# Performance work log

Hardware: AMD Instinct MI355X
Metric: run time of the kernel (lower is better)

## Reference

```python
import jax, jax.numpy as jnp
import numpy as np

B, L, D_MODEL = 4, 2048, 512
N_HEAD, D_K, D_V = 8, 64, 64
RANK = 20


def tt_linear(x, g1, g2, g3, g4, b):
    # TT-matrix linear: input modes (4,4,8,4), output modes (4,4,8,4), ranks [1,20,20,20,1]
    Bx, Lx, _ = x.shape
    t = x.reshape(Bx * Lx, 4, 4, 8, 4)
    t = jnp.einsum('bwxyz,wou->bxyzou', t, g1[0])        # g1: [1,m1,n1,r1]
    t = jnp.einsum('bxyzou,uxpv->byzopv', t, g2)         # g2: [r1,m2,n2,r2]
    t = jnp.einsum('byzopv,vyqw->bzopqw', t, g3)         # g3: [r2,m3,n3,r3]
    t = jnp.einsum('bzopqw,wzs->bopqs', t, g4[..., 0])   # g4: [r3,m4,n4,1]
    return t.reshape(Bx, Lx, -1) + b


def setup_inputs() -> dict:
    key = jax.random.key(0)
    ks = jax.random.split(key, 8)
    scale = jnp.float32(0.15)
    inp = {}
    for name, kk in zip(['wq', 'wk', 'wv', 'fc'], ks[:4]):
        sub = jax.random.split(kk, 4)
        inp[name + '_g1'] = jax.random.normal(sub[0], (1, 4, 4, RANK), jnp.float32) * scale
        inp[name + '_g2'] = jax.random.normal(sub[1], (RANK, 4, 4, RANK), jnp.float32) * scale
        inp[name + '_g3'] = jax.random.normal(sub[2], (RANK, 8, 8, RANK), jnp.float32) * scale
        inp[name + '_g4'] = jax.random.normal(sub[3], (RANK, 4, 4, 1), jnp.float32) * scale
        inp[name + '_b'] = jnp.zeros((D_MODEL,), jnp.float32)
    inp['q'] = jax.random.normal(ks[4], (B, L, D_MODEL), jnp.float32)
    inp['k'] = jax.random.normal(ks[5], (B, L, D_MODEL), jnp.float32)
    inp['v'] = jax.random.normal(ks[6], (B, L, D_MODEL), jnp.float32)
    inp['ln_g'] = jnp.ones((D_MODEL,), jnp.float32)
    inp['ln_b'] = jnp.zeros((D_MODEL,), jnp.float32)
    return inp


def reference(q, k, v,
              wq_g1, wq_g2, wq_g3, wq_g4, wq_b,
              wk_g1, wk_g2, wk_g3, wk_g4, wk_b,
              wv_g1, wv_g2, wv_g3, wv_g4, wv_b,
              fc_g1, fc_g2, fc_g3, fc_g4, fc_b,
              ln_g, ln_b):
    Bx, Lq, _ = q.shape
    residual = q
    qh = tt_linear(q, wq_g1, wq_g2, wq_g3, wq_g4, wq_b).reshape(Bx, Lq, N_HEAD, D_K).transpose(0, 2, 1, 3)
    kh = tt_linear(k, wk_g1, wk_g2, wk_g3, wk_g4, wk_b).reshape(Bx, Lq, N_HEAD, D_K).transpose(0, 2, 1, 3)
    vh = tt_linear(v, wv_g1, wv_g2, wv_g3, wv_g4, wv_b).reshape(Bx, Lq, N_HEAD, D_V).transpose(0, 2, 1, 3)
    temp = jnp.sqrt(jnp.float32(D_K))
    attn = jnp.einsum('bhqd,bhkd->bhqk', qh / temp, kh)  # explicit [B,H,L,L] scores
    attn = jax.nn.softmax(attn, axis=-1)
    o = jnp.einsum('bhqk,bhkd->bhqd', attn, vh)
    o = o.transpose(0, 2, 1, 3).reshape(Bx, Lq, N_HEAD * D_V)
    out = tt_linear(o, fc_g1, fc_g2, fc_g3, fc_g4, fc_b) + residual
    mu = out.mean(-1, keepdims=True)
    var = out.var(-1, keepdims=True)
    out = (out - mu) / jnp.sqrt(var + 1e-12) * ln_g + ln_b
    return (out, attn)
```

## Files before the change

### kernel.cpp

```cpp
#include <hip/hip_runtime.h>
#include <hip/hip_bf16.h>
#include <math.h>

#define BB 4
#define LL 2048
#define DM 512
#define NH 8
#define DK 64
#define RANK 20

typedef __attribute__((ext_vector_type(8))) short short8;
typedef __attribute__((ext_vector_type(4))) short short4b;
typedef __attribute__((ext_vector_type(4))) float f32x4;
typedef __hip_bfloat16 bf16;

__device__ inline short to_bf(float x) {
    bf16 h = __float2bfloat16(x);
    return *reinterpret_cast<short*>(&h);
}
__device__ inline unsigned pk2(float lo, float hi) {
    return ((unsigned)(unsigned short)to_bf(hi) << 16) |
           (unsigned)(unsigned short)to_bf(lo);
}

struct BwArgs {
    const float* g1[4]; const float* g2[4]; const float* g3[4]; const float* g4[4];
    bf16* wt[4];
};
__global__ __launch_bounds__(256) void build_w_kernel(BwArgs args)
{
    int s4 = blockIdx.y;
    const float* __restrict__ g1 = args.g1[s4];
    const float* __restrict__ g2 = args.g2[s4];
    const float* __restrict__ g3 = args.g3[s4];
    const float* __restrict__ g4 = args.g4[s4];
    bf16* __restrict__ Wt = args.wt[s4];

    int idx = blockIdx.x * 256 + threadIdx.x;
    if (idx >= 4*4*8*4*4*8) return;
    int q = idx & 7; int t = idx >> 3;
    int p = t & 3;  t >>= 2;
    int o = t & 3;  t >>= 2;
    int y = t & 7;  t >>= 3;
    int x = t & 3;  t >>= 2;
    int w = t & 3;

    float c[RANK];
    for (int v = 0; v < RANK; ++v) c[v] = 0.f;
    for (int u = 0; u < RANK; ++u) {
        float a = g1[(w*4 + o)*RANK + u];
        const float* g2p = g2 + ((u*4 + x)*4 + p)*RANK;
        for (int v = 0; v < RANK; ++v) c[v] += a * g2p[v];
    }
    float d[RANK];
    for (int r = 0; r < RANK; ++r) d[r] = 0.f;
    for (int v = 0; v < RANK; ++v) {
        float cv = c[v];
        const float* g3p = g3 + ((v*8 + y)*8 + q)*RANK;
        for (int r = 0; r < RANK; ++r) d[r] += cv * g3p[r];
    }
    for (int z = 0; z < 4; ++z) {
        for (int s = 0; s < 4; ++s) {
            float acc = 0.f;
            for (int r = 0; r < RANK; ++r) acc += d[r] * g4[(r*4 + z)*4 + s];
            int i = ((w*4 + x)*8 + y)*4 + z;
            int j = ((o*4 + p)*8 + q)*4 + s;
            Wt[(size_t)j*DM + i] = __float2bfloat16(acc);
        }
    }
}

struct CvtArgs { const float* src[3]; bf16* dst[3]; };
__global__ __launch_bounds__(256) void cvt_kernel(CvtArgs args)
{
    int a = blockIdx.y;
    const float* __restrict__ s = args.src[a];
    bf16* __restrict__ d = args.dst[a];
    size_t i = ((size_t)blockIdx.x * 256 + threadIdx.x) * 8;
    float4 v0 = *(const float4*)&s[i];
    float4 v1 = *(const float4*)&s[i + 4];
    short8 h;
    h[0] = to_bf(v0.x); h[1] = to_bf(v0.y); h[2] = to_bf(v0.z); h[3] = to_bf(v0.w);
    h[4] = to_bf(v1.x); h[5] = to_bf(v1.y); h[6] = to_bf(v1.z); h[7] = to_bf(v1.w);
    *(short8*)&d[i] = h;
}

#define GEMM_CORE64(Ap, Bp)                                                        \
    f32x4 acc[2][2] = {};                                                          \
    for (int k0 = 0; k0 < DM; k0 += 32) {                                          \
        short8 a[2], b[2];                                                         \
        _Pragma("unroll")                                                          \
        for (int mt = 0; mt < 2; ++mt)                                             \
            a[mt] = *(const short8*)&Ap[(size_t)(mt*16 + l15)*DM + k0 + l4*8];     \
        _Pragma("unroll")                                                          \
        for (int nt = 0; nt < 2; ++nt)                                             \
            b[nt] = *(const short8*)&Bp[(size_t)(nt*16 + l15)*DM + k0 + l4*8];     \
        _Pragma("unroll")                                                          \
        for (int mt = 0; mt < 2; ++mt)                                             \
            _Pragma("unroll")                                                      \
            for (int nt = 0; nt < 2; ++nt)                                         \
                acc[mt][nt] = __builtin_amdgcn_mfma_f32_16x16x32_bf16(             \
                    a[mt], b[nt], acc[mt][nt], 0, 0, 0);                           \
    }

struct QkvArgs {
    const bf16* A[3]; const bf16* W[3]; const float* bias[3];
    bf16* outQ; bf16* outK; bf16* outV;
};
__global__ __launch_bounds__(256) void gemm_qkv_kernel(QkvArgs args)
{
    int z = blockIdx.z;
    const bf16* __restrict__ A  = args.A[z];
    const bf16* __restrict__ Wt = args.W[z];
    const float* __restrict__ bias = args.bias[z];

    int m0 = blockIdx.x * 64, n0 = blockIdx.y * 64;
    int t = threadIdx.x, lane = t & 63, wave = t >> 6;
    int l15 = lane & 15, l4 = lane >> 4;
    int wm = wave >> 1, wn = wave & 1;
    const bf16* Ap = A  + (size_t)(m0 + wm*32)*DM;
    const bf16* Bp = Wt + (size_t)(n0 + wn*32)*DM;

    GEMM_CORE64(Ap, Bp)

    if (z < 2) {
        bf16* __restrict__ out = (z == 0) ? args.outQ : args.outK;
        float oscale = (z == 0) ? 0.18033688f : 1.0f;
        #pragma unroll
        for (int mt = 0; mt < 2; ++mt) {
            #pragma unroll
            for (int r = 0; r < 4; ++r) {
                int m = m0 + wm*32 + mt*16 + l4*4 + r;
                int l = m & (LL-1), bb = m >> 11;
                #pragma unroll
                for (int nt = 0; nt < 2; ++nt) {
                    int n = n0 + wn*32 + nt*16 + l15;
                    int h = n >> 6, d = n & 63;
                    float val = (acc[mt][nt][r] + bias[n]) * oscale;
                    out[(((size_t)(bb*NH + h))*LL + l)*DK + d] = __float2bfloat16(val);
                }
            }
        }
    } else {
        #pragma unroll
        for (int mt = 0; mt < 2; ++mt) {
            int mbase = m0 + wm*32 + mt*16 + l4*4;
            int l = mbase & (LL-1), bb = mbase >> 11;
            #pragma unroll
            for (int nt = 0; nt < 2; ++nt) {
                int n = n0 + wn*32 + nt*16 + l15;
                int h = n >> 6, d = n & 63;
                float bv = bias[n];
                short4b h4;
                #pragma unroll
                for (int r = 0; r < 4; ++r) h4[r] = to_bf(acc[mt][nt][r] + bv);
                *(short4b*)&args.outV[((size_t)(bb*NH + h)*DK + d)*LL + l] = h4;
            }
        }
    }
}

__global__ __launch_bounds__(256) void gemm_fc_kernel(
    const bf16* __restrict__ A, const bf16* __restrict__ Wt,
    const float* __restrict__ bias, float* __restrict__ out)
{
    int m0 = blockIdx.x * 64, n0 = blockIdx.y * 64;
    int t = threadIdx.x, lane = t & 63, wave = t >> 6;
    int l15 = lane & 15, l4 = lane >> 4;
    int wm = wave >> 1, wn = wave & 1;
    const bf16* Ap = A  + (size_t)(m0 + wm*32)*DM;
    const bf16* Bp = Wt + (size_t)(n0 + wn*32)*DM;

    GEMM_CORE64(Ap, Bp)

    #pragma unroll
    for (int mt = 0; mt < 2; ++mt) {
        #pragma unroll
        for (int r = 0; r < 4; ++r) {
            int m = m0 + wm*32 + mt*16 + l4*4 + r;
            #pragma unroll
            for (int nt = 0; nt < 2; ++nt) {
                int n = n0 + wn*32 + nt*16 + l15;
                out[(size_t)m*DM + n] = acc[mt][nt][r] + bias[n];
            }
        }
    }
}

__global__ __launch_bounds__(256, 2) void attn_a_kernel(
    const bf16* __restrict__ Qh, const bf16* __restrict__ Kh,
    const bf16* __restrict__ Vt, float* __restrict__ invl_g,
    bf16* __restrict__ O)
{
    __shared__ __align__(16) bf16 Ks[128*64];
    __shared__ __align__(16) bf16 Ps[4][32*128];
    __shared__ float invlS[4][32];

    int qt = blockIdx.x, bh = blockIdx.y;
    int q0 = qt * 128;
    int t = threadIdx.x, lane = t & 63, wave = t >> 6;
    int l15 = lane & 15, l4 = lane >> 4;
    int qr0 = wave * 32;

    const bf16* Qp = Qh + ((size_t)bh * LL + q0 + qr0) * DK;
    const bf16* Kp = Kh + (size_t)bh * LL * DK;
    const bf16* Vp = Vt + (size_t)bh * DK * LL;

    short8 aq0[2], aq1[2];
    #pragma unroll
    for (int f = 0; f < 2; ++f) {
        aq0[f] = *(const short8*)&Qp[(size_t)(f*16 + l15)*DK + l4*8];
        aq1[f] = *(const short8*)&Qp[(size_t)(f*16 + l15)*DK + 32 + l4*8];
    }

    int srow = t >> 3, sseg = t & 7;
    int swr = (l15 & 7) << 4;

    float lsum[2] = {0.f, 0.f};
    f32x4 o_acc[2][4] = {};

    for (int kc = 0; kc < LL; kc += 128) {
        #pragma unroll
        for (int i = 0; i < 4; ++i) {
            int row = srow + i*32;
            int off = (sseg*16) ^ ((row & 7) << 4);
            *(short8*)&Ks[row*64 + (off >> 1)] =
                *(const short8*)&Kp[(size_t)(kc + row)*DK + sseg*8];
        }
        __syncthreads();

        short8 vf[16];
        #pragma unroll
        for (int kt = 0; kt < 4; ++kt)
            #pragma unroll
            for (int dt = 0; dt < 4; ++dt)
                vf[kt*4 + dt] =
                    *(const short8*)&Vp[(size_t)(dt*16 + l15)*LL + kc + kt*32 + l4*8];

        #pragma unroll
        for (int ct = 0; ct < 8; ++ct) {
            int rb = (ct*16 + l15) * 64;
            short8 k0f = *(const short8*)&Ks[rb + (((l4*16) ^ swr) >> 1)];
            short8 k1f = *(const short8*)&Ks[rb + (((64 + l4*16) ^ swr) >> 1)];
            #pragma unroll
            for (int f = 0; f < 2; ++f) {
                f32x4 s = {0.f, 0.f, 0.f, 0.f};
                s = __builtin_amdgcn_mfma_f32_16x16x32_bf16(k0f, aq0[f], s, 0, 0, 0);
                s = __builtin_amdgcn_mfma_f32_16x16x32_bf16(k1f, aq1[f], s, 0, 0, 0);
                float p0 = exp2f(s[0]), p1 = exp2f(s[1]);
                float p2 = exp2f(s[2]), p3 = exp2f(s[3]);
                lsum[f] += (p0 + p1) + (p2 + p3);
                uint2 w2;
                w2.x = pk2(p0, p1);
                w2.y = pk2(p2, p3);
                int kb = (ct*32 + l4*8) ^ swr;
                *(uint2*)((char*)&Ps[wave][(f*16 + l15)*128] + kb) = w2;
            }
        }

        #pragma unroll
        for (int f = 0; f < 2; ++f)
            #pragma unroll
            for (int kt = 0; kt < 4; ++kt) {
                short8 a = *(const short8*)
                    &Ps[wave][(f*16 + l15)*128 + (((kt*64 + l4*16) ^ swr) >> 1)];
                #pragma unroll
                for (int dt = 0; dt < 4; ++dt)
                    o_acc[f][dt] = __builtin_amdgcn_mfma_f32_16x16x32_bf16(
                        a, vf[kt*4 + dt], o_acc[f][dt], 0, 0, 0);
            }
        __syncthreads();
    }

    #pragma unroll
    for (int f = 0; f < 2; ++f) {
        float ss = lsum[f];
        ss += __shfl_xor(ss, 16);
        ss += __shfl_xor(ss, 32);
        float inv = 1.0f / ss;
        if (l4 == 0) {
            invl_g[(size_t)bh * LL + q0 + qr0 + f*16 + l15] = inv;
            invlS[wave][f*16 + l15] = inv;
        }
    }

    int bb = bh >> 3, h = bh & 7;
    #pragma unroll
    for (int f = 0; f < 2; ++f) {
        f32x4 iv = *(f32x4*)&invlS[wave][f*16 + l4*4];
        #pragma unroll
        for (int dt = 0; dt < 4; ++dt)
            #pragma unroll
            for (int r = 0; r < 4; ++r) {
                int row = q0 + qr0 + f*16 + l4*4 + r;
                O[((size_t)bb * LL + row) * DM + h*DK + dt*16 + l15] =
                    __float2bfloat16(o_acc[f][dt][r] * iv[r]);
            }
    }
}

__global__ __launch_bounds__(256, 4) void attn_p_kernel(
    const bf16* __restrict__ Qh, const bf16* __restrict__ Kh,
    const float* __restrict__ invl_g, float* __restrict__ attn)
{
    __shared__ __align__(16) bf16 Ks[256*64];

    int ko = blockIdx.x, qt = blockIdx.y, bh = blockIdx.z;
    int kc0 = ko * 256, q0 = qt * 64;
    int t = threadIdx.x, lane = t & 63, wave = t >> 6;
    int l15 = lane & 15, l4 = lane >> 4;
    int qr0 = wave * 16;

    const bf16* Qp = Qh + ((size_t)bh * LL + q0 + qr0) * DK;
    const bf16* Kp = Kh + ((size_t)bh * LL + kc0) * DK;

    short8 bq0 = *(const short8*)&Qp[(size_t)l15*DK + l4*8];
    short8 bq1 = *(const short8*)&Qp[(size_t)l15*DK + 32 + l4*8];
    float inv = invl_g[(size_t)bh * LL + q0 + qr0 + l15];

    #pragma unroll
    for (int g = 0; g < 8; ++g) {
        int off = (g*16) ^ ((t & 7) << 4);
        *(short8*)&Ks[t*64 + (off >> 1)] =
            *(const short8*)&Kp[(size_t)t*DK + g*8];
    }
    __syncthreads();

    int swr = (l15 & 7) << 4;
    float* ap = attn + ((size_t)bh * LL + q0 + qr0 + l15) * LL + kc0;

    #pragma unroll 4
    for (int ct = 0; ct < 16; ++ct) {
        int rb = (ct*16 + l15) * 64;
        short8 a0 = *(const short8*)&Ks[rb + (((l4*16) ^ swr) >> 1)];
        short8 a1 = *(const short8*)&Ks[rb + (((64 + l4*16) ^ swr) >> 1)];
        f32x4 s = {0.f, 0.f, 0.f, 0.f};
        s = __builtin_amdgcn_mfma_f32_16x16x32_bf16(a0, bq0, s, 0, 0, 0);
        s = __builtin_amdgcn_mfma_f32_16x16x32_bf16(a1, bq1, s, 0, 0, 0);
        float4 o;
        o.x = exp2f(s[0]) * inv;
        o.y = exp2f(s[1]) * inv;
        o.z = exp2f(s[2]) * inv;
        o.w = exp2f(s[3]) * inv;
        *(float4*)&ap[ct*16 + l4*4] = o;
    }
}

__global__ __launch_bounds__(256) void ln_kernel(
    const float* __restrict__ Y, const float* __restrict__ Res,
    const float* __restrict__ g, const float* __restrict__ bta,
    float* __restrict__ out)
{
    int row = blockIdx.x;
    int t = threadIdx.x;
    const float* yp = Y  + (size_t)row*DM;
    const float* rp = Res + (size_t)row*DM;
    float v0 = yp[t]       + rp[t];
    float v1 = yp[t + 256] + rp[t + 256];
    float s1 = v0 + v1;
    float s2 = v0*v0 + v1*v1;
    __shared__ float red1[4], red2[4];
    #pragma unroll
    for (int off = 32; off >= 1; off >>= 1) {
        s1 += __shfl_xor(s1, off);
        s2 += __shfl_xor(s2, off);
    }
    int w = t >> 6;
    if ((t & 63) == 0) { red1[w] = s1; red2[w] = s2; }
    __syncthreads();
    float mu = (red1[0]+red1[1]+red1[2]+red1[3]) * (1.0f/DM);
    float ms = (red2[0]+red2[1]+red2[2]+red2[3]) * (1.0f/DM);
    float inv = rsqrtf(ms - mu*mu + 1e-12f);
    out[(size_t)row*DM + t]       = (v0 - mu)*inv*g[t]       + bta[t];
    out[(size_t)row*DM + t + 256] = (v1 - mu)*inv*g[t + 256] + bta[t + 256];
}

extern "C" void kernel_launch(void* const* d_in, const int* in_sizes, int n_in,
                              void* d_out, int out_size, void* d_ws, size_t ws_size,
                              hipStream_t stream)
{
    const float* G[4][5];
    for (int s = 0; s < 4; ++s)
        for (int i = 0; i < 5; ++i)
            G[s][i] = (const float*)d_in[s*5 + i];
    const float* q   = (const float*)d_in[20];
    const float* k   = (const float*)d_in[21];
    const float* v   = (const float*)d_in[22];
    const float* lng = (const float*)d_in[23];
    const float* lnb = (const float*)d_in[24];

    float* out  = (float*)d_out;
    float* attn = out + (size_t)BB*LL*DM;

    const size_t NTOK = (size_t)BB*LL*DM;
    bf16* wt  = (bf16*)d_ws;
    bf16* qbf = wt + 4*(size_t)DM*DM;
    bf16* kbf = qbf + NTOK;
    bf16* vbf = kbf + NTOK;
    bf16* qh  = vbf + NTOK;
    bf16* kh  = qh + NTOK;
    bf16* vt  = kh + NTOK;
    bf16* o   = vt + NTOK;
    float* y  = (float*)(o + NTOK);
    float* invl = y + NTOK;

    BwArgs bw;
    for (int s = 0; s < 4; ++s) {
        bw.g1[s] = G[s][0]; bw.g2[s] = G[s][1];
        bw.g3[s] = G[s][2]; bw.g4[s] = G[s][3];
        bw.wt[s] = wt + (size_t)s*DM*DM;
    }
    build_w_kernel<<<dim3(64, 4), 256, 0, stream>>>(bw);

    CvtArgs cv;
    cv.src[0] = q; cv.src[1] = k; cv.src[2] = v;
    cv.dst[0] = qbf; cv.dst[1] = kbf; cv.dst[2] = vbf;
    cvt_kernel<<<dim3(NTOK/(256*8), 3), 256, 0, stream>>>(cv);

    QkvArgs qa;
    qa.A[0] = qbf; qa.A[1] = kbf; qa.A[2] = vbf;
    qa.W[0] = wt; qa.W[1] = wt + (size_t)DM*DM; qa.W[2] = wt + 2*(size_t)DM*DM;
    qa.bias[0] = G[0][4]; qa.bias[1] = G[1][4]; qa.bias[2] = G[2][4];
    qa.outQ = qh; qa.outK = kh; qa.outV = vt;
    gemm_qkv_kernel<<<dim3(BB*LL/64, DM/64, 3), 256, 0, stream>>>(qa);

    attn_a_kernel<<<dim3(LL/128, BB*NH), 256, 0, stream>>>(qh, kh, vt, invl, o);

    attn_p_kernel<<<dim3(LL/256, LL/64, BB*NH), 256, 0, stream>>>(qh, kh, invl, attn);

    gemm_fc_kernel<<<dim3(BB*LL/64, DM/64), 256, 0, stream>>>(
        o, wt + 3*(size_t)DM*DM, G[3][4], y);
    ln_kernel<<<BB*LL, 256, 0, stream>>>(y, q, lng, lnb, out);
}
```

Measured before the change: 388.0 us.

## Fuse fp32-to-bf16 conversion into QKV GEMM and double-buffer K tiles in attention

Removes the separate cvt_kernel and has the QKV GEMM load fp32 q/k/v directly, converting to bf16 in registers before the MFMA. This drops a full read/write pass over three activation tensors and one launch, at the cost of each GEMM block reading twice as many input bytes (and re-reading them across the 8 N-tiles). The attention kernel also double-buffers the K tile in shared memory, prefetching the next chunk into registers while computing the current one. That removes one barrier per iteration but doubles K LDS usage and raises register pressure.

```diff
diff --git a/kernel.cpp b/kernel.cpp
--- a/kernel.cpp
+++ b/kernel.cpp
@@ -70,47 +70,14 @@
     }
 }
 
-struct CvtArgs { const float* src[3]; bf16* dst[3]; };
-__global__ __launch_bounds__(256) void cvt_kernel(CvtArgs args)
-{
-    int a = blockIdx.y;
-    const float* __restrict__ s = args.src[a];
-    bf16* __restrict__ d = args.dst[a];
-    size_t i = ((size_t)blockIdx.x * 256 + threadIdx.x) * 8;
-    float4 v0 = *(const float4*)&s[i];
-    float4 v1 = *(const float4*)&s[i + 4];
-    short8 h;
-    h[0] = to_bf(v0.x); h[1] = to_bf(v0.y); h[2] = to_bf(v0.z); h[3] = to_bf(v0.w);
-    h[4] = to_bf(v1.x); h[5] = to_bf(v1.y); h[6] = to_bf(v1.z); h[7] = to_bf(v1.w);
-    *(short8*)&d[i] = h;
-}
-
-#define GEMM_CORE64(Ap, Bp)                                                        \
-    f32x4 acc[2][2] = {};                                                          \
-    for (int k0 = 0; k0 < DM; k0 += 32) {                                          \
-        short8 a[2], b[2];                                                         \
-        _Pragma("unroll")                                                          \
-        for (int mt = 0; mt < 2; ++mt)                                             \
-            a[mt] = *(const short8*)&Ap[(size_t)(mt*16 + l15)*DM + k0 + l4*8];     \
-        _Pragma("unroll")                                                          \
-        for (int nt = 0; nt < 2; ++nt)                                             \
-            b[nt] = *(const short8*)&Bp[(size_t)(nt*16 + l15)*DM + k0 + l4*8];     \
-        _Pragma("unroll")                                                          \
-        for (int mt = 0; mt < 2; ++mt)                                             \
-            _Pragma("unroll")                                                      \
-            for (int nt = 0; nt < 2; ++nt)                                         \
-                acc[mt][nt] = __builtin_amdgcn_mfma_f32_16x16x32_bf16(             \
-                    a[mt], b[nt], acc[mt][nt], 0, 0, 0);                           \
-    }
-
 struct QkvArgs {
-    const bf16* A[3]; const bf16* W[3]; const float* bias[3];
+    const float* A[3]; const bf16* W[3]; const float* bias[3];
     bf16* outQ; bf16* outK; bf16* outV;
 };
 __global__ __launch_bounds__(256) void gemm_qkv_kernel(QkvArgs args)
 {
     int z = blockIdx.z;
-    const bf16* __restrict__ A  = args.A[z];
+    const float* __restrict__ A  = args.A[z];
     const bf16* __restrict__ Wt = args.W[z];
     const float* __restrict__ bias = args.bias[z];
 
@@ -118,10 +85,32 @@
     int t = threadIdx.x, lane = t & 63, wave = t >> 6;
     int l15 = lane & 15, l4 = lane >> 4;
     int wm = wave >> 1, wn = wave & 1;
-    const bf16* Ap = A  + (size_t)(m0 + wm*32)*DM;
-    const bf16* Bp = Wt + (size_t)(n0 + wn*32)*DM;
-
-    GEMM_CORE64(Ap, Bp)
+    const float* Ap = A  + (size_t)(m0 + wm*32)*DM;
+    const bf16*  Bp = Wt + (size_t)(n0 + wn*32)*DM;
+
+    f32x4 acc[2][2] = {};
+    for (int k0 = 0; k0 < DM; k0 += 32) {
+        short8 a[2], b[2];
+        #pragma unroll
+        for (int mt = 0; mt < 2; ++mt) {
+            const float* ap = &Ap[(size_t)(mt*16 + l15)*DM + k0 + l4*8];
+            float4 x0 = *(const float4*)ap;
+            float4 x1 = *(const float4*)(ap + 4);
+            short8 af;
+            af[0]=to_bf(x0.x); af[1]=to_bf(x0.y); af[2]=to_bf(x0.z); af[3]=to_bf(x0.w);
+            af[4]=to_bf(x1.x); af[5]=to_bf(x1.y); af[6]=to_bf(x1.z); af[7]=to_bf(x1.w);
+            a[mt] = af;
+        }
+        #pragma unroll
+        for (int nt = 0; nt < 2; ++nt)
+            b[nt] = *(const short8*)&Bp[(size_t)(nt*16 + l15)*DM + k0 + l4*8];
+        #pragma unroll
+        for (int mt = 0; mt < 2; ++mt)
+            #pragma unroll
+            for (int nt = 0; nt < 2; ++nt)
+                acc[mt][nt] = __builtin_amdgcn_mfma_f32_16x16x32_bf16(
+                    a[mt], b[nt], acc[mt][nt], 0, 0, 0);
+    }
 
     if (z < 2) {
         bf16* __restrict__ out = (z == 0) ? args.outQ : args.outK;
@@ -171,7 +160,22 @@
     const bf16* Ap = A  + (size_t)(m0 + wm*32)*DM;
     const bf16* Bp = Wt + (size_t)(n0 + wn*32)*DM;
 
-    GEMM_CORE64(Ap, Bp)
+    f32x4 acc[2][2] = {};
+    for (int k0 = 0; k0 < DM; k0 += 32) {
+        short8 a[2], b[2];
+        #pragma unroll
+        for (int mt = 0; mt < 2; ++mt)
+            a[mt] = *(const short8*)&Ap[(size_t)(mt*16 + l15)*DM + k0 + l4*8];
+        #pragma unroll
+        for (int nt = 0; nt < 2; ++nt)
+            b[nt] = *(const short8*)&Bp[(size_t)(nt*16 + l15)*DM + k0 + l4*8];
+        #pragma unroll
+        for (int mt = 0; mt < 2; ++mt)
+            #pragma unroll
+            for (int nt = 0; nt < 2; ++nt)
+                acc[mt][nt] = __builtin_amdgcn_mfma_f32_16x16x32_bf16(
+                    a[mt], b[nt], acc[mt][nt], 0, 0, 0);
+    }
 
     #pragma unroll
     for (int mt = 0; mt < 2; ++mt) {
@@ -192,7 +196,7 @@
     const bf16* __restrict__ Vt, float* __restrict__ invl_g,
     bf16* __restrict__ O)
 {
-    __shared__ __align__(16) bf16 Ks[128*64];
+    __shared__ __align__(16) bf16 Ks[2][128*64];
     __shared__ __align__(16) bf16 Ps[4][32*128];
     __shared__ float invlS[4][32];
 
@@ -215,20 +219,29 @@
 
     int srow = t >> 3, sseg = t & 7;
     int swr = (l15 & 7) << 4;
+    int soff = (sseg*16) ^ ((srow & 7) << 4);
 
     float lsum[2] = {0.f, 0.f};
     f32x4 o_acc[2][4] = {};
 
+    short8 kreg[4];
+    #pragma unroll
+    for (int i = 0; i < 4; ++i)
+        kreg[i] = *(const short8*)&Kp[(size_t)(srow + i*32)*DK + sseg*8];
+    #pragma unroll
+    for (int i = 0; i < 4; ++i)
+        *(short8*)&Ks[0][(srow + i*32)*64 + (soff >> 1)] = kreg[i];
+    __syncthreads();
+
     for (int kc = 0; kc < LL; kc += 128) {
-        #pragma unroll
-        for (int i = 0; i < 4; ++i) {
-            int row = srow + i*32;
-            int off = (sseg*16) ^ ((row & 7) << 4);
-            *(short8*)&Ks[row*64 + (off >> 1)] =
-                *(const short8*)&Kp[(size_t)(kc + row)*DK + sseg*8];
-        }
-        __syncthreads();
-
+        int cur = (kc >> 7) & 1;
+        bool more = (kc + 128) < LL;
+
+        if (more) {
+            #pragma unroll
+            for (int i = 0; i < 4; ++i)
+                kreg[i] = *(const short8*)&Kp[(size_t)(kc + 128 + srow + i*32)*DK + sseg*8];
+        }
         short8 vf[16];
         #pragma unroll
         for (int kt = 0; kt < 4; ++kt)
@@ -237,11 +250,12 @@
                 vf[kt*4 + dt] =
                     *(const short8*)&Vp[(size_t)(dt*16 + l15)*LL + kc + kt*32 + l4*8];
 
+        const bf16* Kb = &Ks[cur][0];
         #pragma unroll
         for (int ct = 0; ct < 8; ++ct) {
             int rb = (ct*16 + l15) * 64;
-            short8 k0f = *(const short8*)&Ks[rb + (((l4*16) ^ swr) >> 1)];
-            short8 k1f = *(const short8*)&Ks[rb + (((64 + l4*16) ^ swr) >> 1)];
+            short8 k0f = *(const short8*)&Kb[rb + (((l4*16) ^ swr) >> 1)];
+            short8 k1f = *(const short8*)&Kb[rb + (((64 + l4*16) ^ swr) >> 1)];
             #pragma unroll
             for (int f = 0; f < 2; ++f) {
                 f32x4 s = {0.f, 0.f, 0.f, 0.f};
@@ -269,6 +283,12 @@
                     o_acc[f][dt] = __builtin_amdgcn_mfma_f32_16x16x32_bf16(
                         a, vf[kt*4 + dt], o_acc[f][dt], 0, 0, 0);
             }
+
+        if (more) {
+            #pragma unroll
+            for (int i = 0; i < 4; ++i)
+                *(short8*)&Ks[cur ^ 1][(srow + i*32)*64 + (soff >> 1)] = kreg[i];
+        }
         __syncthreads();
     }
 
@@ -394,10 +414,7 @@
 
     const size_t NTOK = (size_t)BB*LL*DM;
     bf16* wt  = (bf16*)d_ws;
-    bf16* qbf = wt + 4*(size_t)DM*DM;
-    bf16* kbf = qbf + NTOK;
-    bf16* vbf = kbf + NTOK;
-    bf16* qh  = vbf + NTOK;
+    bf16* qh  = wt + 4*(size_t)DM*DM;
     bf16* kh  = qh + NTOK;
     bf16* vt  = kh + NTOK;
     bf16* o   = vt + NTOK;
@@ -412,13 +429,8 @@
     }
     build_w_kernel<<<dim3(64, 4), 256, 0, stream>>>(bw);
 
-    CvtArgs cv;
-    cv.src[0] = q; cv.src[1] = k; cv.src[2] = v;
-    cv.dst[0] = qbf; cv.dst[1] = kbf; cv.dst[2] = vbf;
-    cvt_kernel<<<dim3(NTOK/(256*8), 3), 256, 0, stream>>>(cv);
-
     QkvArgs qa;
-    qa.A[0] = qbf; qa.A[1] = kbf; qa.A[2] = vbf;
+    qa.A[0] = q; qa.A[1] = k; qa.A[2] = v;
     qa.W[0] = wt; qa.W[1] = wt + (size_t)DM*DM; qa.W[2] = wt + 2*(size_t)DM*DM;
     qa.bias[0] = G[0][4]; qa.bias[1] = G[1][4]; qa.bias[2] = G[2][4];
     qa.outQ = qh; qa.outK = kh; qa.outV = vt;
```

After: 403.9 us. +4.1%, slower.

## Halve attention P shared buffer and raise occupancy to four blocks per CU

Applied to the files above, without the earlier changes.

The per-wave P staging buffer is cut to 16 rows. The second 16-row fragment's probabilities are held in registers and written to shared memory only after the first fragment's PV matmul has consumed the buffer. V fragments are loaded from global memory inside the PV loop instead of being preloaded into 16 registers, and launch bounds rise to 4 blocks per CU. The goal is to cut LDS and register use so more blocks run concurrently. The cost is V being read from global twice per tile and less latency hiding for those loads.

```diff
diff --git a/kernel.cpp b/kernel.cpp
--- a/kernel.cpp
+++ b/kernel.cpp
@@ -187,13 +187,13 @@
     }
 }
 
-__global__ __launch_bounds__(256, 2) void attn_a_kernel(
+__global__ __launch_bounds__(256, 4) void attn_a_kernel(
     const bf16* __restrict__ Qh, const bf16* __restrict__ Kh,
     const bf16* __restrict__ Vt, float* __restrict__ invl_g,
     bf16* __restrict__ O)
 {
     __shared__ __align__(16) bf16 Ks[128*64];
-    __shared__ __align__(16) bf16 Ps[4][32*128];
+    __shared__ __align__(16) bf16 Ps[4][16*128];
     __shared__ float invlS[4][32];
 
     int qt = blockIdx.x, bh = blockIdx.y;
@@ -218,6 +218,7 @@
 
     float lsum[2] = {0.f, 0.f};
     f32x4 o_acc[2][4] = {};
+    char* PsRow = (char*)&Ps[wave][l15*128];
 
     for (int kc = 0; kc < LL; kc += 128) {
         #pragma unroll
@@ -229,46 +230,64 @@
         }
         __syncthreads();
 
-        short8 vf[16];
-        #pragma unroll
-        for (int kt = 0; kt < 4; ++kt)
-            #pragma unroll
-            for (int dt = 0; dt < 4; ++dt)
-                vf[kt*4 + dt] =
-                    *(const short8*)&Vp[(size_t)(dt*16 + l15)*LL + kc + kt*32 + l4*8];
-
+        uint2 preg[8];
         #pragma unroll
         for (int ct = 0; ct < 8; ++ct) {
             int rb = (ct*16 + l15) * 64;
             short8 k0f = *(const short8*)&Ks[rb + (((l4*16) ^ swr) >> 1)];
             short8 k1f = *(const short8*)&Ks[rb + (((64 + l4*16) ^ swr) >> 1)];
-            #pragma unroll
-            for (int f = 0; f < 2; ++f) {
+            int kb = (ct*32 + l4*8) ^ swr;
+            {
                 f32x4 s = {0.f, 0.f, 0.f, 0.f};
-                s = __builtin_amdgcn_mfma_f32_16x16x32_bf16(k0f, aq0[f], s, 0, 0, 0);
-                s = __builtin_amdgcn_mfma_f32_16x16x32_bf16(k1f, aq1[f], s, 0, 0, 0);
+                s = __builtin_amdgcn_mfma_f32_16x16x32_bf16(k0f, aq0[0], s, 0, 0, 0);
+                s = __builtin_amdgcn_mfma_f32_16x16x32_bf16(k1f, aq1[0], s, 0, 0, 0);
                 float p0 = exp2f(s[0]), p1 = exp2f(s[1]);
                 float p2 = exp2f(s[2]), p3 = exp2f(s[3]);
-                lsum[f] += (p0 + p1) + (p2 + p3);
-                uint2 w2;
-                w2.x = pk2(p0, p1);
-                w2.y = pk2(p2, p3);
-                int kb = (ct*32 + l4*8) ^ swr;
-                *(uint2*)((char*)&Ps[wave][(f*16 + l15)*128] + kb) = w2;
-            }
-        }
-
-        #pragma unroll
-        for (int f = 0; f < 2; ++f)
-            #pragma unroll
-            for (int kt = 0; kt < 4; ++kt) {
-                short8 a = *(const short8*)
-                    &Ps[wave][(f*16 + l15)*128 + (((kt*64 + l4*16) ^ swr) >> 1)];
-                #pragma unroll
-                for (int dt = 0; dt < 4; ++dt)
-                    o_acc[f][dt] = __builtin_amdgcn_mfma_f32_16x16x32_bf16(
-                        a, vf[kt*4 + dt], o_acc[f][dt], 0, 0, 0);
-            }
+                lsum[0] += (p0 + p1) + (p2 + p3);
+                uint2 w2; w2.x = pk2(p0, p1); w2.y = pk2(p2, p3);
+                *(uint2*)(PsRow + kb) = w2;
+            }
+            {
+                f32x4 s = {0.f, 0.f, 0.f, 0.f};
+                s = __builtin_amdgcn_mfma_f32_16x16x32_bf16(k0f, aq0[1], s, 0, 0, 0);
+                s = __builtin_amdgcn_mfma_f32_16x16x32_bf16(k1f, aq1[1], s, 0, 0, 0);
+                float p0 = exp2f(s[0]), p1 = exp2f(s[1]);
+                float p2 = exp2f(s[2]), p3 = exp2f(s[3]);
+                lsum[1] += (p0 + p1) + (p2 + p3);
+                preg[ct].x = pk2(p0, p1);
+                preg[ct].y = pk2(p2, p3);
+            }
+        }
+
+        #pragma unroll
+        for (int kt = 0; kt < 4; ++kt) {
+            short8 a = *(const short8*)
+                &Ps[wave][l15*128 + (((kt*64 + l4*16) ^ swr) >> 1)];
+            #pragma unroll
+            for (int dt = 0; dt < 4; ++dt) {
+                short8 b = *(const short8*)&Vp[(size_t)(dt*16 + l15)*LL + kc + kt*32 + l4*8];
+                o_acc[0][dt] = __builtin_amdgcn_mfma_f32_16x16x32_bf16(
+                    a, b, o_acc[0][dt], 0, 0, 0);
+            }
+        }
+
+        #pragma unroll
+        for (int ct = 0; ct < 8; ++ct) {
+            int kb = (ct*32 + l4*8) ^ swr;
+            *(uint2*)(PsRow + kb) = preg[ct];
+        }
+
+        #pragma unroll
+        for (int kt = 0; kt < 4; ++kt) {
+            short8 a = *(const short8*)
+                &Ps[wave][l15*128 + (((kt*64 + l4*16) ^ swr) >> 1)];
+            #pragma unroll
+            for (int dt = 0; dt < 4; ++dt) {
+                short8 b = *(const short8*)&Vp[(size_t)(dt*16 + l15)*LL + kc + kt*32 + l4*8];
+                o_acc[1][dt] = __builtin_amdgcn_mfma_f32_16x16x32_bf16(
+                    a, b, o_acc[1][dt], 0, 0, 0);
+            }
+        }
         __syncthreads();
     }
 
```

Result: slower. 484.1 us (+24.8%).
